# Optimization experiments

Measured on AMD Instinct MI355X. Metric: run time of the kernel, lower is better.

The kernel has to match this reference:

```python
import jax, jax.numpy as jnp
import numpy as np

N_NODES = 100000
N_EDGES = 3200000
IN_DIM = 128
HID_DIM = 64
OUT_DIM = 2
N_GRAPHS = 512


def setup_inputs() -> dict:
    key = jax.random.key(0)
    ks = jax.random.split(key, 8)
    x = jax.random.normal(ks[0], (N_NODES, IN_DIM), dtype=jnp.float32)
    edge_index = jax.random.randint(ks[1], (2, N_EDGES), 0, N_NODES, dtype=jnp.int64)
    batch = jnp.sort(jax.random.randint(ks[2], (N_NODES,), 0, N_GRAPHS, dtype=jnp.int64))
    # GCNConv params (glorot-ish scale)
    W_gcn = jax.random.normal(ks[3], (IN_DIM, HID_DIM), dtype=jnp.float32) / np.sqrt(IN_DIM)
    b_gcn = jnp.zeros((HID_DIM,), dtype=jnp.float32)
    # MLP params: Linear(hid,hid) -> ReLU -> Linear(hid,out)
    W1 = jax.random.normal(ks[4], (HID_DIM, HID_DIM), dtype=jnp.float32) / np.sqrt(HID_DIM)
    b1 = jnp.zeros((HID_DIM,), dtype=jnp.float32)
    W2 = jax.random.normal(ks[5], (HID_DIM, OUT_DIM), dtype=jnp.float32) / np.sqrt(HID_DIM)
    b2 = jnp.zeros((OUT_DIM,), dtype=jnp.float32)
    return {"x": x, "edge_index": edge_index, "batch": batch,
            "W_gcn": W_gcn, "b_gcn": b_gcn, "W1": W1, "b1": b1, "W2": W2, "b2": b2}


def reference(x, edge_index, batch, W_gcn, b_gcn, W1, b1, W2, b2):
    n = x.shape[0]
    # --- GCNConv: add self-loops, symmetric normalization, aggregate, transform ---
    self_loop = jnp.arange(n, dtype=edge_index.dtype)
    row = jnp.concatenate([edge_index[0], self_loop])  # source nodes
    col = jnp.concatenate([edge_index[1], self_loop])  # target nodes
    deg = jax.ops.segment_sum(jnp.ones_like(col, dtype=x.dtype), col, num_segments=n)
    dinv = jnp.where(deg > 0, jax.lax.rsqrt(deg), 0.0)
    norm = dinv[row] * dinv[col]                       # (E+N,)
    xw = x @ W_gcn                                     # (N, hid) transform first (in_dim > hid)
    msg = xw[row] * norm[:, None]                      # gather + scale
    z = jax.ops.segment_sum(msg, col, num_segments=n) + b_gcn  # scatter-add
    z = jax.nn.relu(z)
    # --- global mean pool over graphs ---
    sums = jax.ops.segment_sum(z, batch, num_segments=N_GRAPHS)          # (G, hid)
    cnts = jax.ops.segment_sum(jnp.ones((n,), z.dtype), batch, num_segments=N_GRAPHS)
    g = sums / jnp.maximum(cnts, 1.0)[:, None]
    # --- MLP -> sigmoid ---
    h = jax.nn.relu(g @ W1 + b1)
    return jax.nn.sigmoid(h @ W2 + b2)                 # (G, out_dim)
```

## Files before the change

### kernel.cpp

```cpp
#include <hip/hip_runtime.h>

#define N_NODES 100000
#define N_EDGES 3200000
#define IN_DIM 128
#define HID_DIM 64
#define OUT_DIM 2
#define N_GRAPHS 512

#define BSHIFT 6
#define NBK 1563
#define NB3 256
#define EPB 12500
#define CAPSHIFT 12
#define LDS_E2 2816
#define ZERO_ROW N_NODES

__device__ inline unsigned short f2bf(float f) {
    union { float f; unsigned int i; } v; v.f = f;
    unsigned int r = v.i + 0x7fffu + ((v.i >> 16) & 1u);
    return (unsigned short)(r >> 16);
}

typedef __attribute__((ext_vector_type(8))) short bf16x8;
typedef __attribute__((ext_vector_type(4))) float f32x4;
typedef __attribute__((ext_vector_type(2))) float f32x2;

__global__ __launch_bounds__(1024) void k_init(int* __restrict__ cnt_g) {
    int i = blockIdx.x * 1024 + threadIdx.x;
    if (i < NBK) cnt_g[i] = 0;
}

__global__ __launch_bounds__(512) void k_bin(const int* __restrict__ row,
                                             const int* __restrict__ col,
                                             int* __restrict__ cnt_g,
                                             int* __restrict__ binned,
                                             float* __restrict__ gsum,
                                             float* __restrict__ gcnt,
                                             unsigned char* __restrict__ xws) {
    __shared__ int h[NBK];
    __shared__ int cur[NBK];
    __shared__ int colbuf[EPB];
    int b = blockIdx.x;
    for (int i = threadIdx.x; i < NBK; i += 512) { h[i] = 0; cur[i] = 0; }
    if (threadIdx.x < 128) gsum[b * 128 + threadIdx.x] = 0.f;
    if (b == 0) {
        gcnt[threadIdx.x] = 0.f;
        if (threadIdx.x >= 496)
            ((int*)(xws + (size_t)ZERO_ROW * HID_DIM))[threadIdx.x - 496] = 0;
    }
    __syncthreads();
    int s = b * EPB;
    for (int it = 0, i = s + threadIdx.x; i < s + EPB; i += 512, ++it) {
        int c = col[i];
        colbuf[it * 512 + threadIdx.x] = c;
        atomicAdd(&h[c >> BSHIFT], 1);
    }
    __syncthreads();
    for (int i = threadIdx.x; i < NBK; i += 512) {
        int hv = h[i];
        if (hv) h[i] = (i << CAPSHIFT) + atomicAdd(&cnt_g[i], hv);
    }
    __syncthreads();
    for (int it = 0, i = s + threadIdx.x; i < s + EPB; i += 512, ++it) {
        int c = colbuf[it * 512 + threadIdx.x];
        int r = row[i];
        int bk = c >> BSHIFT;
        int rk = atomicAdd(&cur[bk], 1);
        binned[h[bk] + rk] = ((c & 63) << 17) | r;
    }
}

__global__ __launch_bounds__(256) void k_gemm(const float* __restrict__ x,
                                              const float* __restrict__ Wg,
                                              const int* __restrict__ cnt_g,
                                              const int* __restrict__ binned,
                                              unsigned char* __restrict__ xws) {
    __shared__ unsigned short wb[16][64][8];
    __shared__ int cnt[64];

    if (threadIdx.x < 64) cnt[threadIdx.x] = 0;
    for (int idx = threadIdx.x; idx < 1024; idx += 256) {
        int f = idx >> 6, l = idx & 63;
        int ks = f >> 2, nt = f & 3;
        int n = (l & 15) + (nt << 4);
        int kbase = (ks << 5) + ((l >> 4) << 3);
        unsigned short tmp[8];
#pragma unroll
        for (int j = 0; j < 8; j++)
            tmp[j] = f2bf(Wg[(kbase + j) * HID_DIM + n]);
        *(bf16x8*)&wb[f][l][0] = *(const bf16x8*)tmp;
    }
    __syncthreads();

    int bkt = blockIdx.x;
    int m = cnt_g[bkt];
    for (int i = threadIdx.x; i < m; i += 256)
        atomicAdd(&cnt[binned[(bkt << CAPSHIFT) + i] >> 17], 1);

    int wave = threadIdx.x >> 6;
    int lane = threadIdx.x & 63;
    int q = lane >> 4, nn = lane & 15;

    bf16x8 bfrag[4][4];
#pragma unroll
    for (int ks = 0; ks < 4; ks++)
#pragma unroll
        for (int nt = 0; nt < 4; nt++)
            bfrag[ks][nt] = *(const bf16x8*)&wb[ks * 4 + nt][lane][0];

    int node0 = bkt * 64 + wave * 16;
    int arow = node0 + nn;
    if (arow > N_NODES - 1) arow = N_NODES - 1;
    const float* xrow = x + (size_t)arow * IN_DIM + (q << 3);

    f32x4 acc[4] = {{0.f,0.f,0.f,0.f},{0.f,0.f,0.f,0.f},
                    {0.f,0.f,0.f,0.f},{0.f,0.f,0.f,0.f}};
#pragma unroll
    for (int ks = 0; ks < 4; ks++) {
        float4 xa = *(const float4*)(xrow + ks * 32);
        float4 xb_ = *(const float4*)(xrow + ks * 32 + 4);
        bf16x8 af;
        af[0] = (short)f2bf(xa.x); af[1] = (short)f2bf(xa.y);
        af[2] = (short)f2bf(xa.z); af[3] = (short)f2bf(xa.w);
        af[4] = (short)f2bf(xb_.x); af[5] = (short)f2bf(xb_.y);
        af[6] = (short)f2bf(xb_.z); af[7] = (short)f2bf(xb_.w);
#pragma unroll
        for (int nt = 0; nt < 4; nt++)
            acc[nt] = __builtin_amdgcn_mfma_f32_16x16x32_bf16(af, bfrag[ks][nt], acc[nt], 0, 0, 0);
    }
    __syncthreads();

#pragma unroll
    for (int r = 0; r < 4; r++) {
        int lrow = wave * 16 + q * 4 + r;
        int mrow = bkt * 64 + lrow;
        if (mrow < N_NODES) {
            float dn = rsqrtf((float)cnt[lrow] + 1.0f);
            int p01 = __builtin_amdgcn_cvt_pk_fp8_f32(acc[0][r] * dn, acc[1][r] * dn, 0, false);
            int p23 = __builtin_amdgcn_cvt_pk_fp8_f32(acc[2][r] * dn, acc[3][r] * dn, 0, false);
            unsigned char* rp = xws + (size_t)mrow * HID_DIM + nn;
            rp[0]  = (unsigned char)(p01 & 0xff);
            rp[16] = (unsigned char)((p01 >> 8) & 0xff);
            rp[32] = (unsigned char)(p23 & 0xff);
            rp[48] = (unsigned char)((p23 >> 8) & 0xff);
        }
    }
}

__global__ __launch_bounds__(512) void k_aggrf(const unsigned char* __restrict__ xws,
                                               const int* __restrict__ binned,
                                               const int* __restrict__ cnt_g,
                                               const int* __restrict__ batch,
                                               const float* __restrict__ bg,
                                               float* __restrict__ gsum,
                                               float* __restrict__ gcnt) {
    int bkt = blockIdx.x;
    int nbase = bkt << BSHIFT;
    int nnodes = N_NODES - nbase; if (nnodes > 64) nnodes = 64;
    int m = cnt_g[bkt];
    int base = bkt << CAPSHIFT;

    __shared__ int cnt[64];
    __shared__ int lptr[65];
    __shared__ int cur[64];
    __shared__ int sb[64];
    __shared__ float gcl[8];
    __shared__ alignas(16) int srt[LDS_E2];
    __shared__ float pool[8][4][64];

    if (threadIdx.x < 64) {
        int n = nbase + threadIdx.x;
        cnt[threadIdx.x] = 0;
        sb[threadIdx.x]  = (threadIdx.x < nnodes) ? batch[n] : 0;
        cur[threadIdx.x] = 0;
    }
    if (threadIdx.x < 8) gcl[threadIdx.x] = 0.f;
    for (int t = threadIdx.x; t < 8 * 4 * 64; t += 512)
        ((float*)pool)[t] = 0.f;
    __syncthreads();

    for (int i = threadIdx.x; i < m; i += 512)
        atomicAdd(&cnt[binned[base + i] >> 17], 1);
    __syncthreads();

    if (threadIdx.x < 64) {
        int v = (threadIdx.x < nnodes) ? ((cnt[threadIdx.x] + 8) & ~7) : 0;
        int run = v;
#pragma unroll
        for (int off = 1; off < 64; off <<= 1) {
            int t = __shfl_up(run, off);
            if (threadIdx.x >= off) run += t;
        }
        lptr[threadIdx.x + 1] = run;
        if (threadIdx.x == 0) lptr[0] = 0;
    }
    __syncthreads();
    int tot = lptr[64]; if (tot > LDS_E2) tot = LDS_E2;
    for (int i = threadIdx.x; i < tot; i += 512) srt[i] = ZERO_ROW << 6;
    __syncthreads();
    if (threadIdx.x < nnodes) {
        int p = lptr[threadIdx.x] + cnt[threadIdx.x];
        if (p < LDS_E2) srt[p] = (nbase + threadIdx.x) << 6;
        int sl = sb[threadIdx.x] - sb[0];
        if (sl < 8) atomicAdd(&gcl[sl], 1.0f);
        else atomicAdd(&gcnt[sb[threadIdx.x]], 1.0f);
    }
    for (int i = threadIdx.x; i < m; i += 512) {
        int pk = binned[base + i];
        int nid = pk >> 17;
        int rk = atomicAdd(&cur[nid], 1);
        int pos = lptr[nid] + rk;
        if (pos < LDS_E2) srt[pos] = (pk & 0x1FFFF) << 6;
    }
    __syncthreads();

    int wave = threadIdx.x >> 6;
    int lane = threadIdx.x & 63;
    int sub = lane >> 4;
    int lc  = lane & 15;
    int l4  = lc << 2;
    const unsigned char* xbl = xws + l4;
    int g0 = sb[0];
    float4 bia = ((const float4*)bg)[lc];

#pragma unroll
    for (int r = 0; r < 2; r++) {
        int ln = wave * 8 + sub * 2 + r;
        int valid = (ln < nnodes);
        int s0 = valid ? lptr[ln] : 0;
        int e0 = valid ? lptr[ln + 1] : 0;
        if (s0 > LDS_E2) s0 = LDS_E2;
        if (e0 > LDS_E2) e0 = LDS_E2;
        f32x2 al0 = {0.f,0.f}, ah0 = {0.f,0.f};
        f32x2 al1 = {0.f,0.f}, ah1 = {0.f,0.f};
        for (int i = s0; i < e0; i += 8) {
            int4 ra = *(const int4*)&srt[i];
            int4 rb = *(const int4*)&srt[i + 4];
            unsigned int d0 = *(const unsigned int*)(xbl + ra.x);
            unsigned int d1 = *(const unsigned int*)(xbl + ra.y);
            unsigned int d2 = *(const unsigned int*)(xbl + ra.z);
            unsigned int d3 = *(const unsigned int*)(xbl + ra.w);
            unsigned int d4 = *(const unsigned int*)(xbl + rb.x);
            unsigned int d5 = *(const unsigned int*)(xbl + rb.y);
            unsigned int d6 = *(const unsigned int*)(xbl + rb.z);
            unsigned int d7 = *(const unsigned int*)(xbl + rb.w);
            f32x2 p;
            p = __builtin_amdgcn_cvt_pk_f32_fp8(d0, false); al0 += p;
            p = __builtin_amdgcn_cvt_pk_f32_fp8(d0, true);  ah0 += p;
            p = __builtin_amdgcn_cvt_pk_f32_fp8(d1, false); al1 += p;
            p = __builtin_amdgcn_cvt_pk_f32_fp8(d1, true);  ah1 += p;
            p = __builtin_amdgcn_cvt_pk_f32_fp8(d2, false); al0 += p;
            p = __builtin_amdgcn_cvt_pk_f32_fp8(d2, true);  ah0 += p;
            p = __builtin_amdgcn_cvt_pk_f32_fp8(d3, false); al1 += p;
            p = __builtin_amdgcn_cvt_pk_f32_fp8(d3, true);  ah1 += p;
            p = __builtin_amdgcn_cvt_pk_f32_fp8(d4, false); al0 += p;
            p = __builtin_amdgcn_cvt_pk_f32_fp8(d4, true);  ah0 += p;
            p = __builtin_amdgcn_cvt_pk_f32_fp8(d5, false); al1 += p;
            p = __builtin_amdgcn_cvt_pk_f32_fp8(d5, true);  ah1 += p;
            p = __builtin_amdgcn_cvt_pk_f32_fp8(d6, false); al0 += p;
            p = __builtin_amdgcn_cvt_pk_f32_fp8(d6, true);  ah0 += p;
            p = __builtin_amdgcn_cvt_pk_f32_fp8(d7, false); al1 += p;
            p = __builtin_amdgcn_cvt_pk_f32_fp8(d7, true);  ah1 += p;
        }
        f32x2 alo = al0 + al1, ahi = ah0 + ah1;
        int slot = 99;
        float4 val;
        if (valid) {
            float dn = rsqrtf((float)cnt[ln] + 1.0f);
            val.x = fmaxf(alo[0] * dn + bia.x, 0.f);
            val.y = fmaxf(alo[1] * dn + bia.y, 0.f);
            val.z = fmaxf(ahi[0] * dn + bia.z, 0.f);
            val.w = fmaxf(ahi[1] * dn + bia.w, 0.f);
            slot = sb[ln] - g0;
        }
#pragma unroll
        for (int ss = 0; ss < 4; ss++) {
            if (sub == ss && slot < 4) {
                float4* pp = (float4*)&pool[wave][slot][l4];
                float4 pv = *pp;
                pv.x += val.x; pv.y += val.y; pv.z += val.z; pv.w += val.w;
                *pp = pv;
            }
        }
        if (slot >= 4 && slot < 99) {
            float* gp = &gsum[sb[ln] * HID_DIM + l4];
            atomicAdd(gp + 0, val.x); atomicAdd(gp + 1, val.y);
            atomicAdd(gp + 2, val.z); atomicAdd(gp + 3, val.w);
        }
    }
    __syncthreads();

    if (threadIdx.x < 8) {
        float c = gcl[threadIdx.x];
        if (c != 0.f) atomicAdd(&gcnt[g0 + threadIdx.x], c);
    }
    for (int t = threadIdx.x; t < 4 * 64; t += 512) {
        int slot = t >> 6, j = t & 63;
        float v = 0.f;
#pragma unroll
        for (int w2 = 0; w2 < 8; w2++) v += pool[w2][slot][j];
        if (v != 0.f) atomicAdd(&gsum[(g0 + slot) * HID_DIM + j], v);
    }
}

__global__ __launch_bounds__(64) void k_mlp(const float* __restrict__ gsum,
                                            const float* __restrict__ gcnt,
                                            const float* __restrict__ W1,
                                            const float* __restrict__ b1,
                                            const float* __restrict__ W2,
                                            const float* __restrict__ b2,
                                            float* __restrict__ out) {
    int g = blockIdx.x;
    int j = threadIdx.x;
    float cnt = fmaxf(gcnt[g], 1.0f);

    __shared__ float gs[64];
    __shared__ float hs[64];
    gs[j] = gsum[g * 64 + j] / cnt;
    __syncthreads();

    float h = b1[j];
    for (int k = 0; k < 64; k++) h += gs[k] * W1[k * 64 + j];
    hs[j] = fmaxf(h, 0.f);
    __syncthreads();

    if (j < OUT_DIM) {
        float o = b2[j];
        for (int k = 0; k < 64; k++) o += hs[k] * W2[k * OUT_DIM + j];
        out[g * OUT_DIM + j] = 1.f / (1.f + expf(-o));
    }
}

extern "C" void kernel_launch(void* const* d_in, const int* in_sizes, int n_in,
                              void* d_out, int out_size, void* d_ws, size_t ws_size,
                              hipStream_t stream) {
    const float* x   = (const float*)d_in[0];
    const int* eidx  = (const int*)d_in[1];
    const int* batch = (const int*)d_in[2];
    const float* Wg  = (const float*)d_in[3];
    const float* bg  = (const float*)d_in[4];
    const float* W1  = (const float*)d_in[5];
    const float* b1  = (const float*)d_in[6];
    const float* W2  = (const float*)d_in[7];
    const float* b2  = (const float*)d_in[8];
    float* out = (float*)d_out;

    char* w = (char*)d_ws;
    unsigned char* xws = (unsigned char*)w;     w += (size_t)(N_NODES + 1) * HID_DIM;
    int*   binned  = (int*)w;                   w += ((size_t)NBK << CAPSHIFT) * 4;
    int*   cnt_g   = (int*)w;                   w += NBK * 4;
    float* gsum    = (float*)w;                 w += N_GRAPHS * HID_DIM * 4;
    float* gcnt    = (float*)w;                 w += N_GRAPHS * 4;

    const int* rowp = eidx;
    const int* colp = eidx + N_EDGES;

    k_init<<<2, 1024, 0, stream>>>(cnt_g);
    k_bin<<<NB3, 512, 0, stream>>>(rowp, colp, cnt_g, binned, gsum, gcnt, xws);
    k_gemm<<<NBK, 256, 0, stream>>>(x, Wg, cnt_g, binned, xws);
    k_aggrf<<<NBK, 512, 0, stream>>>(xws, binned, cnt_g, batch, bg, gsum, gcnt);
    k_mlp<<<N_GRAPHS, 64, 0, stream>>>(gsum, gcnt, W1, b1, W2, b2, out);
}
```

Measured before the change: 202.0 us.

## Split binning into more blocks, reuse gemm degree counts in aggregation

The binning kernel now runs 1024 blocks of 3125 edges instead of 256 blocks of 12500. It drops the LDS column buffer and re-reads col from global memory in the second pass, which should raise occupancy and parallelism at the cost of a second col read. Zeroing of gsum, gcnt and the zero row moves into an expanded init kernel. The per-node degree counts already computed in k_gemm are written to a new degs buffer, so k_aggrf no longer rescans binned entries with LDS atomics to recount degrees.

```diff
diff --git a/kernel.cpp b/kernel.cpp
--- a/kernel.cpp
+++ b/kernel.cpp
@@ -9,8 +9,8 @@
 
 #define BSHIFT 6
 #define NBK 1563
-#define NB3 256
-#define EPB 12500
+#define NBB 1024
+#define EPB2 3125
 #define CAPSHIFT 12
 #define LDS_E2 2816
 #define ZERO_ROW N_NODES
@@ -25,44 +25,42 @@
 typedef __attribute__((ext_vector_type(4))) float f32x4;
 typedef __attribute__((ext_vector_type(2))) float f32x2;
 
-__global__ __launch_bounds__(1024) void k_init(int* __restrict__ cnt_g) {
-    int i = blockIdx.x * 1024 + threadIdx.x;
-    if (i < NBK) cnt_g[i] = 0;
+__global__ __launch_bounds__(1024) void k_init(float* __restrict__ gsum,
+                                               int* __restrict__ cnt_g,
+                                               float* __restrict__ gcnt,
+                                               unsigned char* __restrict__ xws) {
+    int b = blockIdx.x, t = threadIdx.x;
+    if (b < 32) {
+        gsum[b * 1024 + t] = 0.f;
+    } else if (b < 34) {
+        int j = (b - 32) * 1024 + t;
+        if (j < NBK) cnt_g[j] = 0;
+    } else {
+        if (t < N_GRAPHS) gcnt[t] = 0.f;
+        if (t >= 1008)
+            ((int*)(xws + (size_t)ZERO_ROW * HID_DIM))[t - 1008] = 0;
+    }
 }
 
 __global__ __launch_bounds__(512) void k_bin(const int* __restrict__ row,
                                              const int* __restrict__ col,
                                              int* __restrict__ cnt_g,
-                                             int* __restrict__ binned,
-                                             float* __restrict__ gsum,
-                                             float* __restrict__ gcnt,
-                                             unsigned char* __restrict__ xws) {
+                                             int* __restrict__ binned) {
     __shared__ int h[NBK];
     __shared__ int cur[NBK];
-    __shared__ int colbuf[EPB];
-    int b = blockIdx.x;
     for (int i = threadIdx.x; i < NBK; i += 512) { h[i] = 0; cur[i] = 0; }
-    if (threadIdx.x < 128) gsum[b * 128 + threadIdx.x] = 0.f;
-    if (b == 0) {
-        gcnt[threadIdx.x] = 0.f;
-        if (threadIdx.x >= 496)
-            ((int*)(xws + (size_t)ZERO_ROW * HID_DIM))[threadIdx.x - 496] = 0;
-    }
-    __syncthreads();
-    int s = b * EPB;
-    for (int it = 0, i = s + threadIdx.x; i < s + EPB; i += 512, ++it) {
-        int c = col[i];
-        colbuf[it * 512 + threadIdx.x] = c;
-        atomicAdd(&h[c >> BSHIFT], 1);
-    }
+    __syncthreads();
+    int s = blockIdx.x * EPB2, e = s + EPB2;
+    for (int i = s + threadIdx.x; i < e; i += 512)
+        atomicAdd(&h[col[i] >> BSHIFT], 1);
     __syncthreads();
     for (int i = threadIdx.x; i < NBK; i += 512) {
         int hv = h[i];
         if (hv) h[i] = (i << CAPSHIFT) + atomicAdd(&cnt_g[i], hv);
     }
     __syncthreads();
-    for (int it = 0, i = s + threadIdx.x; i < s + EPB; i += 512, ++it) {
-        int c = colbuf[it * 512 + threadIdx.x];
+    for (int i = s + threadIdx.x; i < e; i += 512) {
+        int c = col[i];
         int r = row[i];
         int bk = c >> BSHIFT;
         int rk = atomicAdd(&cur[bk], 1);
@@ -74,6 +72,7 @@
                                               const float* __restrict__ Wg,
                                               const int* __restrict__ cnt_g,
                                               const int* __restrict__ binned,
+                                              int* __restrict__ degs,
                                               unsigned char* __restrict__ xws) {
     __shared__ unsigned short wb[16][64][8];
     __shared__ int cnt[64];
@@ -129,6 +128,8 @@
             acc[nt] = __builtin_amdgcn_mfma_f32_16x16x32_bf16(af, bfrag[ks][nt], acc[nt], 0, 0, 0);
     }
     __syncthreads();
+
+    if (threadIdx.x < 64) degs[bkt * 64 + threadIdx.x] = cnt[threadIdx.x];
 
 #pragma unroll
     for (int r = 0; r < 4; r++) {
@@ -150,6 +151,7 @@
 __global__ __launch_bounds__(512) void k_aggrf(const unsigned char* __restrict__ xws,
                                                const int* __restrict__ binned,
                                                const int* __restrict__ cnt_g,
+                                               const int* __restrict__ degs,
                                                const int* __restrict__ batch,
                                                const float* __restrict__ bg,
                                                float* __restrict__ gsum,
@@ -170,17 +172,13 @@
 
     if (threadIdx.x < 64) {
         int n = nbase + threadIdx.x;
-        cnt[threadIdx.x] = 0;
+        cnt[threadIdx.x] = (threadIdx.x < nnodes) ? degs[bkt * 64 + threadIdx.x] : 0;
         sb[threadIdx.x]  = (threadIdx.x < nnodes) ? batch[n] : 0;
         cur[threadIdx.x] = 0;
     }
     if (threadIdx.x < 8) gcl[threadIdx.x] = 0.f;
     for (int t = threadIdx.x; t < 8 * 4 * 64; t += 512)
         ((float*)pool)[t] = 0.f;
-    __syncthreads();
-
-    for (int i = threadIdx.x; i < m; i += 512)
-        atomicAdd(&cnt[binned[base + i] >> 17], 1);
     __syncthreads();
 
     if (threadIdx.x < 64) {
@@ -349,15 +347,16 @@
     unsigned char* xws = (unsigned char*)w;     w += (size_t)(N_NODES + 1) * HID_DIM;
     int*   binned  = (int*)w;                   w += ((size_t)NBK << CAPSHIFT) * 4;
     int*   cnt_g   = (int*)w;                   w += NBK * 4;
+    int*   degs    = (int*)w;                   w += (size_t)NBK * 64 * 4;
     float* gsum    = (float*)w;                 w += N_GRAPHS * HID_DIM * 4;
     float* gcnt    = (float*)w;                 w += N_GRAPHS * 4;
 
     const int* rowp = eidx;
     const int* colp = eidx + N_EDGES;
 
-    k_init<<<2, 1024, 0, stream>>>(cnt_g);
-    k_bin<<<NB3, 512, 0, stream>>>(rowp, colp, cnt_g, binned, gsum, gcnt, xws);
-    k_gemm<<<NBK, 256, 0, stream>>>(x, Wg, cnt_g, binned, xws);
-    k_aggrf<<<NBK, 512, 0, stream>>>(xws, binned, cnt_g, batch, bg, gsum, gcnt);
+    k_init<<<35, 1024, 0, stream>>>(gsum, cnt_g, gcnt, xws);
+    k_bin<<<NBB, 512, 0, stream>>>(rowp, colp, cnt_g, binned);
+    k_gemm<<<NBK, 256, 0, stream>>>(x, Wg, cnt_g, binned, degs, xws);
+    k_aggrf<<<NBK, 512, 0, stream>>>(xws, binned, cnt_g, degs, batch, bg, gsum, gcnt);
     k_mlp<<<N_GRAPHS, 64, 0, stream>>>(gsum, gcnt, W1, b1, W2, b2, out);
 }
```

Result: slower. 228.9 us (+13.3%).
